# Performance work log

Hardware: AMD Instinct MI355X
Metric: run time of the kernel (lower is better)

## Reference

```python
import jax, jax.numpy as jnp
import numpy as np

B, S, N, CIN = 256, 64, 17, 3
HID, HEADS = 64, 2
OUT, NCLS = 128, 10
LSTM_IN = HID * HEADS * N  # 2176
NEG_SLOPE = 0.2


def setup_inputs() -> dict:
    key = jax.random.key(0)
    ks = iter(jax.random.split(key, 64))
    def p(shape, scale=0.1):
        return jax.random.normal(next(ks), shape, jnp.float32) * scale
    inp = {}
    inp["x"] = jax.random.normal(next(ks), (B, S, N, CIN), jnp.float32)
    inp["edge_index"] = jax.random.randint(next(ks), (2, 64), 0, N, dtype=jnp.int32)
    # 4 GATConv layers: (L0.conv1, L0.conv2, L1.conv1, L1.conv2)
    ins = [CIN, HID * HEADS, HID * HEADS, HID * HEADS]
    for i, cin in enumerate(ins):
        inp[f"gw{i}"] = p((cin, HEADS * HID))
        inp[f"gas{i}"] = p((HEADS, HID))
        inp[f"gad{i}"] = p((HEADS, HID))
        inp[f"gb{i}"] = p((HEADS * HID,))
    for l, ind in enumerate([LSTM_IN, OUT]):
        inp[f"wih{l}"] = p((4 * OUT, ind))
        inp[f"whh{l}"] = p((4 * OUT, OUT))
        inp[f"bih{l}"] = p((4 * OUT,))
        inp[f"bhh{l}"] = p((4 * OUT,))
    inp["attn_w"] = p((1, OUT))
    inp["attn_b"] = p((1,))
    inp["fc_w"] = p((NCLS, OUT))
    inp["fc_b"] = p((NCLS,))
    return inp


def gat_conv(h_in, src, dst, W, a_src, a_dst, b):
    # h_in: [G, N, Cin]; PyG GATConv (concat=True, negative_slope=0.2, self-loops already in src/dst)
    G, n, _ = h_in.shape
    D = W.shape[1] // HEADS
    h = (h_in @ W).reshape(G, n, HEADS, D)            # [G,N,H,D]
    a_s = jnp.einsum('gnhd,hd->gnh', h, a_src)
    a_d = jnp.einsum('gnhd,hd->gnh', h, a_dst)
    e = jax.nn.leaky_relu(a_s[:, src] + a_d[:, dst], NEG_SLOPE)  # [G,E,H]
    m = jnp.full((G, n, HEADS), -1e30, e.dtype).at[:, dst].max(e)
    ex = jnp.exp(e - m[:, dst])
    den = jnp.zeros((G, n, HEADS), e.dtype).at[:, dst].add(ex)
    alpha = ex / (den[:, dst] + 1e-16)
    out = jnp.zeros((G, n, HEADS, D), e.dtype).at[:, dst].add(alpha[..., None] * h[:, src])
    return out.reshape(G, n, HEADS * D) + b


def lstm_layer(x, wih, whh, bih, bhh):
    # x: [B, T, In]; PyTorch gate order i, f, g, o
    Hh = whh.shape[1]
    def step(carry, xt):
        h, c = carry
        g = xt @ wih.T + h @ whh.T + bih + bhh
        i, f, gg, o = jnp.split(g, 4, axis=-1)
        c = jax.nn.sigmoid(f) * c + jax.nn.sigmoid(i) * jnp.tanh(gg)
        h = jax.nn.sigmoid(o) * jnp.tanh(c)
        return (h, c), h
    z = jnp.zeros((x.shape[0], Hh), x.dtype)
    _, hs = jax.lax.scan(step, (z, z), jnp.swapaxes(x, 0, 1))
    return jnp.swapaxes(hs, 0, 1)


def forward(x, edge_index, gw0, gas0, gad0, gb0, gw1, gas1, gad1, gb1,
            gw2, gas2, gad2, gb2, gw3, gas3, gad3, gb3,
            wih0, whh0, bih0, bhh0, wih1, whh1, bih1, bhh1,
            attn_w, attn_b, fc_w, fc_b):
    loops = jnp.arange(N, dtype=edge_index.dtype)
    src = jnp.concatenate([edge_index[0], loops])
    dst = jnp.concatenate([edge_index[1], loops])
    h = x.reshape(B * S, N, CIN)  # all batch*seq graphs in parallel
    h = jax.nn.relu(gat_conv(h, src, dst, gw0, gas0, gad0, gb0))
    h = gat_conv(h, src, dst, gw1, gas1, gad1, gb1)
    h = jax.nn.relu(gat_conv(h, src, dst, gw2, gas2, gad2, gb2))
    h = gat_conv(h, src, dst, gw3, gas3, gad3, gb3)
    lstm_in = h.reshape(B, S, LSTM_IN)
    h1 = lstm_layer(lstm_in, wih0, whh0, bih0, bhh0)
    h2 = lstm_layer(h1, wih1, whh1, bih1, bhh1)
    aw = jax.nn.softmax(jnp.tanh(h2 @ attn_w.T + attn_b), axis=1)  # [B,S,1]
    context = jnp.sum(aw * h2, axis=1)
    return context @ fc_w.T + fc_b


def reference(x, edge_index, gw0, gas0, gad0, gb0, gw1, gas1, gad1, gb1,
              gw2, gas2, gad2, gb2, gw3, gas3, gad3, gb3,
              wih0, whh0, bih0, bhh0, wih1, whh1, bih1, bhh1,
              attn_w, attn_b, fc_w, fc_b):
    return forward(x, edge_index, gw0, gas0, gad0, gb0, gw1, gas1, gad1, gb1,
                   gw2, gas2, gad2, gb2, gw3, gas3, gad3, gb3,
                   wih0, whh0, bih0, bhh0, wih1, whh1, bih1, bhh1,
                   attn_w, attn_b, fc_w, fc_b)
```

## Files before the change

### kernel.cpp

```cpp
#include <hip/hip_runtime.h>
#include <hip/hip_bf16.h>

#define Bb 256
#define Nn_ 17
#define CIN 3
#define HID 64
#define CCH 128
#define Gg 16384
#define Ee 81
#define LSTM_IN 2176
#define OUT_ 128
#define G4 512
#define NCLS 10
#define Tt 64
#define Mg (Gg * Nn_)

typedef unsigned short u16;
typedef unsigned int u32;
typedef __attribute__((ext_vector_type(8))) short bf16x8;
typedef __attribute__((ext_vector_type(4))) float f32x4;

__device__ __forceinline__ u16 f2bf(float f) {
    u32 u = __float_as_uint(f);
    u += 0x7fffu + ((u >> 16) & 1u);
    return (u16)(u >> 16);
}
__device__ __forceinline__ float bflo(u32 v) { return __uint_as_float(v << 16); }
__device__ __forceinline__ float bfhi(u32 v) { return __uint_as_float(v & 0xffff0000u); }

__device__ __forceinline__ void async16(const void* g, void* l) {
    __builtin_amdgcn_global_load_lds((__attribute__((address_space(1))) u32*)g,
                                     (__attribute__((address_space(3))) u32*)l, 16, 0, 0);
}

__global__ void k_setup(const int* __restrict__ edge_index, int* __restrict__ csr) {
    if (threadIdx.x == 0 && blockIdx.x == 0) {
        int* src = csr;
        int* dst = csr + Ee;
        int* off = csr + 2 * Ee;
        int* eid = csr + 2 * Ee + Nn_ + 1;
        for (int e = 0; e < 64; e++) { src[e] = edge_index[e]; dst[e] = edge_index[64 + e]; }
        for (int n = 0; n < Nn_; n++) { src[64 + n] = n; dst[64 + n] = n; }
        int cnt[Nn_];
        for (int n = 0; n < Nn_; n++) cnt[n] = 0;
        for (int e = 0; e < Ee; e++) cnt[dst[e]]++;
        off[0] = 0;
        for (int n = 0; n < Nn_; n++) off[n + 1] = off[n] + cnt[n];
        int pos[Nn_];
        for (int n = 0; n < Nn_; n++) pos[n] = off[n];
        for (int e = 0; e < Ee; e++) eid[pos[dst[e]]++] = e;
    }
}

__global__ void k_convert(const float* __restrict__ in, u16* __restrict__ out, long n) {
    long i = (long)blockIdx.x * 256 + threadIdx.x;
    if (i < n) out[i] = f2bf(in[i]);
}
__global__ void k_convert_t128(const float* __restrict__ in, u16* __restrict__ out) {
    int i = blockIdx.x * 256 + threadIdx.x;
    int n = i >> 7, k = i & 127;
    out[i] = f2bf(in[k * 128 + n]);
}

__global__ __launch_bounds__(256) void k_l0(const float* __restrict__ x,
                                            const float* __restrict__ W0,
                                            const float* __restrict__ gas0,
                                            const float* __restrict__ gad0,
                                            u16* __restrict__ h, float* __restrict__ aux) {
    __shared__ float ws[3 * 128];
    __shared__ float w0a[12];
    const int t = threadIdx.x;
    for (int i = t; i < 384; i += 256) ws[i] = W0[i];
    __syncthreads();
    if (t < 12) {
        int ci = t >> 2, j = t & 3;
        const float* a = (j < 2) ? gas0 : gad0;
        int hh = j & 1;
        float s = 0.f;
        for (int d = 0; d < HID; d++) s += ws[ci * 128 + hh * 64 + d] * a[hh * 64 + d];
        w0a[t] = s;
    }
    __syncthreads();
    const long row = (long)blockIdx.x * 16 + (t >> 4);
    const int c0 = (t & 15) * 8;
    const float x0 = x[row * 3 + 0], x1 = x[row * 3 + 1], x2 = x[row * 3 + 2];
    union { uint4 u; u16 s[8]; } o;
#pragma unroll
    for (int j = 0; j < 8; j++)
        o.s[j] = f2bf(x0 * ws[c0 + j] + x1 * ws[128 + c0 + j] + x2 * ws[256 + c0 + j]);
    *(uint4*)(h + row * 128 + c0) = o.u;
    if ((t & 15) < 4) {
        int j = t & 3;
        aux[row * 4 + j] = x0 * w0a[j] + x1 * w0a[4 + j] + x2 * w0a[8 + j];
    }
}

__global__ __launch_bounds__(256) void k_gemm_gat(u16* __restrict__ HB,
                                                  const u16* __restrict__ Wt,
                                                  const float* __restrict__ a_src,
                                                  const float* __restrict__ a_dst,
                                                  float* __restrict__ aux) {
    __shared__ u16 ldsA[128 * 128];
    __shared__ float avec[128], dvec[128];
    const int t = threadIdx.x;
    const int w = t >> 6, lane = t & 63;
    const int q = lane >> 4, col = lane & 15;
    const long bm = (long)blockIdx.x * 128;
    const int wm = w * 32;

    if (t < 128) avec[t] = a_src[t];
    else dvec[t - 128] = a_dst[t - 128];

#pragma unroll
    for (int i = 0; i < 8; i++) {
        const int slot = (w * 8 + i) * 64 + lane;
        const int r = slot >> 4, cs = slot & 15;
        const int cg = cs ^ (r & 15);
        async16(HB + (bm + r) * 128 + cg * 8, ldsA + (w * 8 + i) * 512);
    }
    __syncthreads();

    f32x4 acc[2][8] = {};
#pragma unroll
    for (int ks = 0; ks < 4; ks++) {
        const int ck = ks * 4 + q;
        bf16x8 af[2];
#pragma unroll
        for (int mt = 0; mt < 2; mt++) {
            const int m = wm + mt * 16 + col;
            af[mt] = *(const bf16x8*)&ldsA[m * 128 + ((ck ^ (m & 15)) << 3)];
        }
#pragma unroll
        for (int nt = 0; nt < 8; nt++) {
            bf16x8 bf = *(const bf16x8*)&Wt[(nt * 16 + col) * 128 + ck * 8];
            acc[0][nt] = __builtin_amdgcn_mfma_f32_16x16x32_bf16(af[0], bf, acc[0][nt], 0, 0, 0);
            acc[1][nt] = __builtin_amdgcn_mfma_f32_16x16x32_bf16(af[1], bf, acc[1][nt], 0, 0, 0);
        }
    }
    __syncthreads();
#pragma unroll
    for (int mt = 0; mt < 2; mt++) {
#pragma unroll
        for (int nt = 0; nt < 8; nt++) {
            const int cg = nt * 16 + col;
#pragma unroll
            for (int r = 0; r < 4; r++) {
                const long rg = bm + wm + mt * 16 + q * 4 + r;
                HB[rg * 128 + cg] = f2bf(acc[mt][nt][r]);
            }
        }
#pragma unroll
        for (int r = 0; r < 4; r++) {
            float s0 = 0.f, s1 = 0.f, d0 = 0.f, d1 = 0.f;
#pragma unroll
            for (int nt = 0; nt < 4; nt++) {
                const float v = acc[mt][nt][r];
                s0 += v * avec[nt * 16 + col];
                d0 += v * dvec[nt * 16 + col];
            }
#pragma unroll
            for (int nt = 4; nt < 8; nt++) {
                const float v = acc[mt][nt][r];
                s1 += v * avec[nt * 16 + col];
                d1 += v * dvec[nt * 16 + col];
            }
#pragma unroll
            for (int o = 1; o < 16; o <<= 1) {
                s0 += __shfl_xor(s0, o);
                s1 += __shfl_xor(s1, o);
                d0 += __shfl_xor(d0, o);
                d1 += __shfl_xor(d1, o);
            }
            if (col == 0) {
                const long rg = bm + wm + mt * 16 + q * 4 + r;
                aux[rg * 4 + 0] = s0;
                aux[rg * 4 + 1] = s1;
                aux[rg * 4 + 2] = d0;
                aux[rg * 4 + 3] = d1;
            }
        }
    }
}

#define GPB 4
__global__ __launch_bounds__(256) void k_gat_attn(u16* __restrict__ h,
                                                  const float* __restrict__ aux,
                                                  const float* __restrict__ bias,
                                                  const int* __restrict__ csr,
                                                  int relu_flag) {
    __shared__ __align__(16) u32 hs[GPB * Nn_ * 64];
    __shared__ float asd[GPB * Nn_ * 4];
    __shared__ float ev[GPB][162];
    __shared__ float mS[GPB][34], dS[GPB][34];
    __shared__ float bvec[128];
    __shared__ int srcS[Ee], dstS[Ee], offS[Nn_ + 1], eidS[Ee];
    const int t = threadIdx.x;
    const long g0 = (long)blockIdx.x * GPB;

    if (t < Ee) { srcS[t] = csr[t]; dstS[t] = csr[Ee + t]; eidS[t] = csr[180 + t]; }
    if (t >= 128 && t < 128 + Nn_ + 1) offS[t - 128] = csr[162 + t - 128];
    if (t < 128) bvec[t] = bias[t];
    {
        const uint4* hg4 = (const uint4*)((const u32*)h + g0 * 1088);
        for (int i = t; i < GPB * Nn_ * 16; i += 256) ((uint4*)hs)[i] = hg4[i];
        const float* ag = aux + g0 * 68;
        for (int i = t; i < GPB * Nn_ * 4; i += 256) asd[i] = ag[i];
    }
    __syncthreads();
    for (int i = t; i < GPB * 162; i += 256) {
        const int g = i / 162, rem = i % 162, e = rem >> 1, hh = rem & 1;
        float v = asd[(g * Nn_ + srcS[e]) * 4 + hh] + asd[(g * Nn_ + dstS[e]) * 4 + 2 + hh];
        ev[g][rem] = (v > 0.f) ? v : 0.2f * v;
    }
    __syncthreads();
    if (t < GPB * 34) {
        const int g = t / 34, rem = t % 34, n = rem >> 1, hh = rem & 1;
        const int p0 = offS[n], p1 = offS[n + 1];
        float m = -1e30f;
        for (int p = p0; p < p1; p++) m = fmaxf(m, ev[g][eidS[p] * 2 + hh]);
        float den = 0.f;
        for (int p = p0; p < p1; p++) den += expf(ev[g][eidS[p] * 2 + hh] - m);
        mS[g][rem] = m;
        dS[g][rem] = den;
    }
    __syncthreads();
    for (int i = t; i < GPB * 162; i += 256) {
        const int g = i / 162, rem = i % 162, e = rem >> 1, hh = rem & 1;
        const int n = dstS[e];
        ev[g][rem] = expf(ev[g][rem] - mS[g][n * 2 + hh]) / (dS[g][n * 2 + hh] + 1e-16f);
    }
    __syncthreads();
    uint4* hgo4 = (uint4*)((u32*)h + g0 * 1088);
    for (int i = t; i < GPB * Nn_ * 16; i += 256) {
        const int g = i / (Nn_ * 16), rem = i % (Nn_ * 16);
        const int n = rem >> 4, cq = rem & 15, hh = cq >> 3;
        const int p0 = offS[n], p1 = offS[n + 1];
        float a[8] = {};
        for (int p = p0; p < p1; p++) {
            const int e = eidS[p];
            const uint4 hv = ((const uint4*)hs)[(g * Nn_ + srcS[e]) * 16 + cq];
            const float al = ev[g][e * 2 + hh];
            a[0] += al * bflo(hv.x); a[1] += al * bfhi(hv.x);
            a[2] += al * bflo(hv.y); a[3] += al * bfhi(hv.y);
            a[4] += al * bflo(hv.z); a[5] += al * bfhi(hv.z);
            a[6] += al * bflo(hv.w); a[7] += al * bfhi(hv.w);
        }
        const int c0 = cq * 8;
#pragma unroll
        for (int m2 = 0; m2 < 8; m2++) {
            a[m2] += bvec[c0 + m2];
            if (relu_flag) a[m2] = fmaxf(a[m2], 0.f);
        }
        uint4 o;
        o.x = (u32)f2bf(a[0]) | ((u32)f2bf(a[1]) << 16);
        o.y = (u32)f2bf(a[2]) | ((u32)f2bf(a[3]) << 16);
        o.z = (u32)f2bf(a[4]) | ((u32)f2bf(a[5]) << 16);
        o.w = (u32)f2bf(a[6]) | ((u32)f2bf(a[7]) << 16);
        hgo4[(g * Nn_ + n) * 16 + cq] = o;
    }
}

__global__ __launch_bounds__(256) void k_gemm_mfma(const u16* __restrict__ A,
                                                   const u16* __restrict__ Bt,
                                                   float* __restrict__ Cm,
                                                   const float* __restrict__ b1,
                                                   const float* __restrict__ b2,
                                                   int K, int ldc) {
    __shared__ u16 ldsA[128 * 64];
    __shared__ u16 ldsB[128 * 64];
    const int w = threadIdx.x >> 6;
    const int lane = threadIdx.x & 63;
    const long bm = (long)blockIdx.x * 128;
    const int bn = blockIdx.y * 128;
    const int wm = (w & 1) * 64, wn = (w >> 1) * 64;
    const int q = lane >> 4, col = lane & 15;
    f32x4 acc[4][4] = {};
    for (int k0 = 0; k0 < K; k0 += 64) {
#pragma unroll
        for (int i = 0; i < 4; i++) {
            const int slot = (w * 4 + i) * 64 + lane;
            const int r = slot >> 3, cs = slot & 7;
            const int cg = cs ^ (r & 7);
            async16(A + (bm + r) * (long)K + k0 + cg * 8, ldsA + (w * 4 + i) * 512);
            async16(Bt + (long)(bn + r) * K + k0 + cg * 8, ldsB + (w * 4 + i) * 512);
        }
        __syncthreads();
#pragma unroll
        for (int kk = 0; kk < 2; kk++) {
            bf16x8 af[4], bfr[4];
#pragma unroll
            for (int mt = 0; mt < 4; mt++) {
                const int m = wm + mt * 16 + col;
                const int cs = (kk * 4 + q) ^ (m & 7);
                af[mt] = *(const bf16x8*)&ldsA[m * 64 + cs * 8];
            }
#pragma unroll
            for (int nt = 0; nt < 4; nt++) {
                const int n = wn + nt * 16 + col;
                const int cs = (kk * 4 + q) ^ (n & 7);
                bfr[nt] = *(const bf16x8*)&ldsB[n * 64 + cs * 8];
            }
#pragma unroll
            for (int mt = 0; mt < 4; mt++)
#pragma unroll
                for (int nt = 0; nt < 4; nt++)
                    acc[mt][nt] = __builtin_amdgcn_mfma_f32_16x16x32_bf16(af[mt], bfr[nt], acc[mt][nt], 0, 0, 0);
        }
        __syncthreads();
    }
#pragma unroll
    for (int mt = 0; mt < 4; mt++)
#pragma unroll
        for (int nt = 0; nt < 4; nt++) {
            const int cg = bn + wn + nt * 16 + col;
            const float bb = b1[cg] + b2[cg];
#pragma unroll
            for (int r = 0; r < 4; r++) {
                const long rg = bm + wm + mt * 16 + q * 4 + r;
                Cm[rg * ldc + cg] = acc[mt][nt][r] + bb;
            }
        }
}

template <int OBF16>
__global__ __launch_bounds__(512, 1) void k_lstm(const float* __restrict__ XW,
                                                 const u16* __restrict__ whhb,
                                                 void* __restrict__ hseq) {
    const int b = blockIdx.x, j = threadIdx.x;
    u32 wp[64];
    const u32* wrow = (const u32*)(whhb + (long)j * OUT_);
#pragma unroll
    for (int k = 0; k < 64; k++) wp[k] = wrow[k];
    __shared__ __align__(16) float h_s[OUT_];
    __shared__ float gate_s[G4];
    float c_r = 0.f;
    if (j < OUT_) h_s[j] = 0.f;
    float xw = XW[((long)b * Tt + 0) * G4 + j];
    const int gate = j >> 7;
    __syncthreads();
    for (int t = 0; t < Tt; t++) {
        float xw_next = 0.f;
        if (t < Tt - 1) xw_next = XW[((long)b * Tt + t + 1) * G4 + j];
        float a0 = xw, a1 = 0.f, a2 = 0.f, a3 = 0.f;
#pragma unroll
        for (int k = 0; k < 32; k += 4) {
            const float4 h0 = ((const float4*)h_s)[k];
            const float4 h1 = ((const float4*)h_s)[k + 1];
            const float4 h2 = ((const float4*)h_s)[k + 2];
            const float4 h3 = ((const float4*)h_s)[k + 3];
            u32 p0 = wp[2 * k], p1 = wp[2 * k + 1];
            a0 += bflo(p0) * h0.x + bfhi(p0) * h0.y + bflo(p1) * h0.z + bfhi(p1) * h0.w;
            p0 = wp[2 * k + 2]; p1 = wp[2 * k + 3];
            a1 += bflo(p0) * h1.x + bfhi(p0) * h1.y + bflo(p1) * h1.z + bfhi(p1) * h1.w;
            p0 = wp[2 * k + 4]; p1 = wp[2 * k + 5];
            a2 += bflo(p0) * h2.x + bfhi(p0) * h2.y + bflo(p1) * h2.z + bfhi(p1) * h2.w;
            p0 = wp[2 * k + 6]; p1 = wp[2 * k + 7];
            a3 += bflo(p0) * h3.x + bfhi(p0) * h3.y + bflo(p1) * h3.z + bfhi(p1) * h3.w;
        }
        const float acc = (a0 + a1) + (a2 + a3);
        gate_s[j] = (gate == 2) ? tanhf(acc) : 1.f / (1.f + expf(-acc));
        __syncthreads();
        if (j < OUT_) {
            const float si = gate_s[j], sf = gate_s[OUT_ + j];
            const float gg = gate_s[2 * OUT_ + j], so = gate_s[3 * OUT_ + j];
            const float c = sf * c_r + si * gg;
            c_r = c;
            const float hh = so * tanhf(c);
            h_s[j] = hh;
            const long idx = ((long)b * Tt + t) * OUT_ + j;
            if (OBF16) ((u16*)hseq)[idx] = f2bf(hh);
            else       ((float*)hseq)[idx] = hh;
        }
        xw = xw_next;
        __syncthreads();
    }
}

__global__ __launch_bounds__(64) void k_attn_fc(const float* __restrict__ h2,
                                                const float* __restrict__ attn_w,
                                                const float* __restrict__ attn_b,
                                                const float* __restrict__ fc_w,
                                                const float* __restrict__ fc_b,
                                                float* __restrict__ out) {
    const int b = blockIdx.x, t = threadIdx.x;
    __shared__ float aw[Tt];
    __shared__ float ctx[OUT_];
    const float* hb = h2 + (long)b * Tt * OUT_;
    float acc = 0.f;
    for (int d = 0; d < OUT_; d++) acc += hb[t * OUT_ + d] * attn_w[d];
    float sc = tanhf(acc + attn_b[0]);
    float m = sc;
#pragma unroll
    for (int o = 32; o > 0; o >>= 1) m = fmaxf(m, __shfl_xor(m, o));
    float ex = expf(sc - m);
    float sum = ex;
#pragma unroll
    for (int o = 32; o > 0; o >>= 1) sum += __shfl_xor(sum, o);
    aw[t] = ex / sum;
    __syncthreads();
    for (int d = t; d < OUT_; d += 64) {
        float c = 0.f;
        for (int tt = 0; tt < Tt; tt++) c += aw[tt] * hb[tt * OUT_ + d];
        ctx[d] = c;
    }
    __syncthreads();
    if (t < NCLS) {
        float o = fc_b[t];
        for (int d = 0; d < OUT_; d++) o += ctx[d] * fc_w[t * OUT_ + d];
        out[b * NCLS + t] = o;
    }
}

extern "C" void kernel_launch(void* const* d_in, const int* in_sizes, int n_in,
                              void* d_out, int out_size, void* d_ws, size_t ws_size,
                              hipStream_t stream) {
    const float* x          = (const float*)d_in[0];
    const int*   edge_index = (const int*)d_in[1];
    const float* gw[4]  = {(const float*)d_in[2], (const float*)d_in[6], (const float*)d_in[10], (const float*)d_in[14]};
    const float* gas[4] = {(const float*)d_in[3], (const float*)d_in[7], (const float*)d_in[11], (const float*)d_in[15]};
    const float* gad[4] = {(const float*)d_in[4], (const float*)d_in[8], (const float*)d_in[12], (const float*)d_in[16]};
    const float* gb[4]  = {(const float*)d_in[5], (const float*)d_in[9], (const float*)d_in[13], (const float*)d_in[17]};
    const float* wih0 = (const float*)d_in[18];
    const float* whh0 = (const float*)d_in[19];
    const float* bih0 = (const float*)d_in[20];
    const float* bhh0 = (const float*)d_in[21];
    const float* wih1 = (const float*)d_in[22];
    const float* whh1 = (const float*)d_in[23];
    const float* bih1 = (const float*)d_in[24];
    const float* bhh1 = (const float*)d_in[25];
    const float* attn_w = (const float*)d_in[26];
    const float* attn_b = (const float*)d_in[27];
    const float* fc_w   = (const float*)d_in[28];
    const float* fc_b   = (const float*)d_in[29];
    float* out = (float*)d_out;
    char* p = (char*)d_ws;

    u16*   hbuf  = (u16*)(p + 0L);
    float* aux   = (float*)(p + 71303168L);
    float* XW0   = (float*)(p + 75759616L);
    float* XW1   = (float*)(p + 109314048L);
    float* h2s   = (float*)(p + 142868480L);
    u16*   h1s   = (u16*)(p + 151257088L);
    u16*   wih0b = (u16*)(p + 155451392L);
    u16*   wih1b = (u16*)(p + 157679616L);
    u16*   whh0b = (u16*)(p + 157810688L);
    u16*   whh1b = (u16*)(p + 157941760L);
    u16*   wt1   = (u16*)(p + 158072832L);
    u16*   wt2   = (u16*)(p + 158105600L);
    u16*   wt3   = (u16*)(p + 158138368L);
    int*   csr   = (int*)(p + 158171136L);

    k_setup<<<1, 1, 0, stream>>>(edge_index, csr);
    k_convert_t128<<<64, 256, 0, stream>>>(gw[1], wt1);
    k_convert_t128<<<64, 256, 0, stream>>>(gw[2], wt2);
    k_convert_t128<<<64, 256, 0, stream>>>(gw[3], wt3);
    k_convert<<<(512 * 2176 + 255) / 256, 256, 0, stream>>>(wih0, wih0b, 512L * 2176);
    k_convert<<<256, 256, 0, stream>>>(wih1, wih1b, 512L * 128);
    k_convert<<<256, 256, 0, stream>>>(whh0, whh0b, 512L * 128);
    k_convert<<<256, 256, 0, stream>>>(whh1, whh1b, 512L * 128);

    k_l0<<<Mg / 16, 256, 0, stream>>>(x, gw[0], gas[0], gad[0], hbuf, aux);
    k_gat_attn<<<Gg / GPB, 256, 0, stream>>>(hbuf, aux, gb[0], csr, 1);
    k_gemm_gat<<<Mg / 128, 256, 0, stream>>>(hbuf, wt1, gas[1], gad[1], aux);
    k_gat_attn<<<Gg / GPB, 256, 0, stream>>>(hbuf, aux, gb[1], csr, 0);
    k_gemm_gat<<<Mg / 128, 256, 0, stream>>>(hbuf, wt2, gas[2], gad[2], aux);
    k_gat_attn<<<Gg / GPB, 256, 0, stream>>>(hbuf, aux, gb[2], csr, 1);
    k_gemm_gat<<<Mg / 128, 256, 0, stream>>>(hbuf, wt3, gas[3], gad[3], aux);
    k_gat_attn<<<Gg / GPB, 256, 0, stream>>>(hbuf, aux, gb[3], csr, 0);

    k_gemm_mfma<<<dim3(Gg / 128, 4), 256, 0, stream>>>(hbuf, wih0b, XW0, bih0, bhh0, LSTM_IN, G4);
    k_lstm<1><<<Bb, 512, 0, stream>>>(XW0, whh0b, h1s);
    k_gemm_mfma<<<dim3(Gg / 128, 4), 256, 0, stream>>>(h1s, wih1b, XW1, bih1, bhh1, OUT_, G4);
    k_lstm<0><<<Bb, 512, 0, stream>>>(XW1, whh1b, h2s);

    k_attn_fc<<<Bb, 64, 0, stream>>>(h2s, attn_w, attn_b, fc_w, fc_b, out);
}
```

Baseline: 733.2 us.

## Merge small weight conversions, parallelize setup loads, pre-unpack LSTM weights to fp32

Six small bf16 conversion launches are merged into one kernel, cutting per-launch overhead. The CSR setup kernel now loads the edge list into shared memory with 128 threads and builds it in local arrays before writing. The LSTM recurrence unpacks the recurrent weights to 128 fp32 registers once, so no bf16 unpacking happens inside the time loop. This doubles per-thread register demand under launch_bounds(512,1), which may cause spills.

Result: faster. 711.2 us (-3.0%).

```diff
diff --git a/kernel.cpp b/kernel.cpp
--- a/kernel.cpp
+++ b/kernel.cpp
@@ -33,22 +33,31 @@
                                      (__attribute__((address_space(3))) u32*)l, 16, 0, 0);
 }
 
-__global__ void k_setup(const int* __restrict__ edge_index, int* __restrict__ csr) {
-    if (threadIdx.x == 0 && blockIdx.x == 0) {
+__global__ __launch_bounds__(128) void k_setup(const int* __restrict__ edge_index,
+                                               int* __restrict__ csr) {
+    __shared__ int eis[128];
+    const int t = threadIdx.x;
+    eis[t] = edge_index[t];
+    __syncthreads();
+    if (t == 0) {
         int* src = csr;
         int* dst = csr + Ee;
         int* off = csr + 2 * Ee;
         int* eid = csr + 2 * Ee + Nn_ + 1;
-        for (int e = 0; e < 64; e++) { src[e] = edge_index[e]; dst[e] = edge_index[64 + e]; }
-        for (int n = 0; n < Nn_; n++) { src[64 + n] = n; dst[64 + n] = n; }
+        int s_[Ee], d_[Ee];
+        for (int e = 0; e < 64; e++) { s_[e] = eis[e]; d_[e] = eis[64 + e]; }
+        for (int n = 0; n < Nn_; n++) { s_[64 + n] = n; d_[64 + n] = n; }
         int cnt[Nn_];
         for (int n = 0; n < Nn_; n++) cnt[n] = 0;
-        for (int e = 0; e < Ee; e++) cnt[dst[e]]++;
-        off[0] = 0;
-        for (int n = 0; n < Nn_; n++) off[n + 1] = off[n] + cnt[n];
+        for (int e = 0; e < Ee; e++) cnt[d_[e]]++;
+        int offl[Nn_ + 1];
+        offl[0] = 0;
+        for (int n = 0; n < Nn_; n++) offl[n + 1] = offl[n] + cnt[n];
         int pos[Nn_];
-        for (int n = 0; n < Nn_; n++) pos[n] = off[n];
-        for (int e = 0; e < Ee; e++) eid[pos[dst[e]]++] = e;
+        for (int n = 0; n < Nn_; n++) pos[n] = offl[n];
+        for (int e = 0; e < Ee; e++) { src[e] = s_[e]; dst[e] = d_[e]; }
+        for (int n = 0; n <= Nn_; n++) off[n] = offl[n];
+        for (int e = 0; e < Ee; e++) eid[pos[d_[e]]++] = e;
     }
 }
 
@@ -56,10 +65,26 @@
     long i = (long)blockIdx.x * 256 + threadIdx.x;
     if (i < n) out[i] = f2bf(in[i]);
 }
-__global__ void k_convert_t128(const float* __restrict__ in, u16* __restrict__ out) {
-    int i = blockIdx.x * 256 + threadIdx.x;
-    int n = i >> 7, k = i & 127;
-    out[i] = f2bf(in[k * 128 + n]);
+
+__global__ __launch_bounds__(256) void k_convert_small(
+    const float* __restrict__ gw1, const float* __restrict__ gw2, const float* __restrict__ gw3,
+    const float* __restrict__ wih1, const float* __restrict__ whh0, const float* __restrict__ whh1,
+    u16* __restrict__ wt1, u16* __restrict__ wt2, u16* __restrict__ wt3,
+    u16* __restrict__ wih1b, u16* __restrict__ whh0b, u16* __restrict__ whh1b) {
+    const int i = blockIdx.x * 256 + threadIdx.x;
+    if (i < 49152) {
+        const int which = i / 16384, r = i % 16384;
+        const float* s = (which == 0) ? gw1 : (which == 1) ? gw2 : gw3;
+        u16* d = (which == 0) ? wt1 : (which == 1) ? wt2 : wt3;
+        const int n = r >> 7, k = r & 127;
+        d[r] = f2bf(s[k * 128 + n]);
+    } else {
+        const int ii = i - 49152;
+        const int which = ii / 65536, r = ii % 65536;
+        const float* s = (which == 0) ? wih1 : (which == 1) ? whh0 : whh1;
+        u16* d = (which == 0) ? wih1b : (which == 1) ? whh0b : whh1b;
+        d[r] = f2bf(s[r]);
+    }
 }
 
 __global__ __launch_bounds__(256) void k_l0(const float* __restrict__ x,
@@ -327,10 +352,16 @@
                                                  const u16* __restrict__ whhb,
                                                  void* __restrict__ hseq) {
     const int b = blockIdx.x, j = threadIdx.x;
-    u32 wp[64];
-    const u32* wrow = (const u32*)(whhb + (long)j * OUT_);
-#pragma unroll
-    for (int k = 0; k < 64; k++) wp[k] = wrow[k];
+    float wf[128];
+    {
+        const u32* wrow = (const u32*)(whhb + (long)j * OUT_);
+#pragma unroll
+        for (int k = 0; k < 64; k++) {
+            const u32 pv = wrow[k];
+            wf[2 * k]     = bflo(pv);
+            wf[2 * k + 1] = bfhi(pv);
+        }
+    }
     __shared__ __align__(16) float h_s[OUT_];
     __shared__ float gate_s[G4];
     float c_r = 0.f;
@@ -343,19 +374,19 @@
         if (t < Tt - 1) xw_next = XW[((long)b * Tt + t + 1) * G4 + j];
         float a0 = xw, a1 = 0.f, a2 = 0.f, a3 = 0.f;
 #pragma unroll
-        for (int k = 0; k < 32; k += 4) {
+        for (int k = 0; k < 8; k++) {
             const float4 h0 = ((const float4*)h_s)[k];
-            const float4 h1 = ((const float4*)h_s)[k + 1];
-            const float4 h2 = ((const float4*)h_s)[k + 2];
-            const float4 h3 = ((const float4*)h_s)[k + 3];
-            u32 p0 = wp[2 * k], p1 = wp[2 * k + 1];
-            a0 += bflo(p0) * h0.x + bfhi(p0) * h0.y + bflo(p1) * h0.z + bfhi(p1) * h0.w;
-            p0 = wp[2 * k + 2]; p1 = wp[2 * k + 3];
-            a1 += bflo(p0) * h1.x + bfhi(p0) * h1.y + bflo(p1) * h1.z + bfhi(p1) * h1.w;
-            p0 = wp[2 * k + 4]; p1 = wp[2 * k + 5];
-            a2 += bflo(p0) * h2.x + bfhi(p0) * h2.y + bflo(p1) * h2.z + bfhi(p1) * h2.w;
-            p0 = wp[2 * k + 6]; p1 = wp[2 * k + 7];
-            a3 += bflo(p0) * h3.x + bfhi(p0) * h3.y + bflo(p1) * h3.z + bfhi(p1) * h3.w;
+            const float4 h1 = ((const float4*)h_s)[8 + k];
+            const float4 h2 = ((const float4*)h_s)[16 + k];
+            const float4 h3 = ((const float4*)h_s)[24 + k];
+            a0 += wf[4 * k + 0] * h0.x + wf[4 * k + 1] * h0.y
+                + wf[4 * k + 2] * h0.z + wf[4 * k + 3] * h0.w;
+            a1 += wf[32 + 4 * k + 0] * h1.x + wf[32 + 4 * k + 1] * h1.y
+                + wf[32 + 4 * k + 2] * h1.z + wf[32 + 4 * k + 3] * h1.w;
+            a2 += wf[64 + 4 * k + 0] * h2.x + wf[64 + 4 * k + 1] * h2.y
+                + wf[64 + 4 * k + 2] * h2.z + wf[64 + 4 * k + 3] * h2.w;
+            a3 += wf[96 + 4 * k + 0] * h3.x + wf[96 + 4 * k + 1] * h3.y
+                + wf[96 + 4 * k + 2] * h3.z + wf[96 + 4 * k + 3] * h3.w;
         }
         const float acc = (a0 + a1) + (a2 + a3);
         gate_s[j] = (gate == 2) ? tanhf(acc) : 1.f / (1.f + expf(-acc));
@@ -450,14 +481,10 @@
     u16*   wt3   = (u16*)(p + 158138368L);
     int*   csr   = (int*)(p + 158171136L);
 
-    k_setup<<<1, 1, 0, stream>>>(edge_index, csr);
-    k_convert_t128<<<64, 256, 0, stream>>>(gw[1], wt1);
-    k_convert_t128<<<64, 256, 0, stream>>>(gw[2], wt2);
-    k_convert_t128<<<64, 256, 0, stream>>>(gw[3], wt3);
+    k_setup<<<1, 128, 0, stream>>>(edge_index, csr);
+    k_convert_small<<<960, 256, 0, stream>>>(gw[1], gw[2], gw[3], wih1, whh0, whh1,
+                                             wt1, wt2, wt3, wih1b, whh0b, whh1b);
     k_convert<<<(512 * 2176 + 255) / 256, 256, 0, stream>>>(wih0, wih0b, 512L * 2176);
-    k_convert<<<256, 256, 0, stream>>>(wih1, wih1b, 512L * 128);
-    k_convert<<<256, 256, 0, stream>>>(whh0, whh0b, 512L * 128);
-    k_convert<<<256, 256, 0, stream>>>(whh1, whh1b, 512L * 128);
 
     k_l0<<<Mg / 16, 256, 0, stream>>>(x, gw[0], gas[0], gad[0], hbuf, aux);
     k_gat_attn<<<Gg / GPB, 256, 0, stream>>>(hbuf, aux, gb[0], csr, 1);
```
